# Kernel tuning notes

Measured on AMD Instinct MI355X. Metric: run time of the kernel, lower is better.

The kernel has to match this reference:

```python
import jax, jax.numpy as jnp
import numpy as np

N_NODES = 50000
N_EDGES = 800000
NFEAT, NHID, NCLASS = 512, 128, 40


def setup_inputs() -> dict:
    key = jax.random.key(0)
    ks = jax.random.split(key, 8)
    stdv1 = 1.0 / np.sqrt(NHID)
    stdv2 = 1.0 / np.sqrt(NCLASS)
    x = jax.random.normal(ks[0], (N_NODES, NFEAT), dtype=jnp.float32)
    W1 = jax.random.uniform(ks[1], (NFEAT, NHID), jnp.float32, -stdv1, stdv1)
    b1 = jax.random.uniform(ks[2], (NHID,), jnp.float32, -stdv1, stdv1)
    W2 = jax.random.uniform(ks[3], (NHID, NCLASS), jnp.float32, -stdv2, stdv2)
    b2 = jax.random.uniform(ks[4], (NCLASS,), jnp.float32, -stdv2, stdv2)
    edge_src = jax.random.randint(ks[5], (N_EDGES,), 0, N_NODES, dtype=jnp.int32)
    edge_dst = jax.random.randint(ks[6], (N_EDGES,), 0, N_NODES, dtype=jnp.int32)
    # normalized adjacency weights (positive, ~1/deg scale)
    edge_w = jax.random.uniform(ks[7], (N_EDGES,), jnp.float32, 0.0, 2.0 / 16.0)
    return {"x": x, "W1": W1, "b1": b1, "W2": W2, "b2": b2,
            "edge_src": edge_src, "edge_dst": edge_dst, "edge_w": edge_w}


def _spmm(edge_src, edge_dst, edge_w, support, n_nodes):
    # out[i] = sum_{e: dst(e)=i} w_e * support[src(e)]  == spmm(adj, support)
    msgs = edge_w[:, None] * support[edge_src]          # [E, F]
    return jax.ops.segment_sum(msgs, edge_dst, num_segments=n_nodes)


def reference(x, W1, b1, W2, b2, edge_src, edge_dst, edge_w):
    # layer 1: dense transform then sparse aggregation, bias, relu
    support = x @ W1                                     # [N, nhid]
    h = _spmm(edge_src, edge_dst, edge_w, support, x.shape[0]) + b1
    h = jax.nn.relu(h)
    # dropout is identity in eval mode
    # layer 2
    support2 = h @ W2                                    # [N, nclass]
    out = _spmm(edge_src, edge_dst, edge_w, support2, x.shape[0]) + b2
    return out
```

## Files before the change

kernel.cpp:

```cpp
#include <hip/hip_runtime.h>
#include <hip/hip_bf16.h>


#define NFEAT 512
#define NHID  128
#define NCLS  40
#define BSH   8
#define SLOTSH 6
#define BSLOT 6144
#define ACHUNK 2048

typedef __attribute__((ext_vector_type(8))) short bf16x8;
typedef __attribute__((ext_vector_type(4))) short bf16x4;
typedef __attribute__((ext_vector_type(4))) float f32x4;
typedef __fp16 cvt16x2 __attribute__((ext_vector_type(2)));
typedef _Float16 h16x2 __attribute__((ext_vector_type(2)));

__device__ inline short f2bf(float f) {
  __hip_bfloat16 b = __float2bfloat16(f);
  return *reinterpret_cast<short*>(&b);
}

__device__ inline bf16x8 cvt8(float4 a, float4 b) {
  bf16x8 r;
  r[0] = f2bf(a.x); r[1] = f2bf(a.y); r[2] = f2bf(a.z); r[3] = f2bf(a.w);
  r[4] = f2bf(b.x); r[5] = f2bf(b.y); r[6] = f2bf(b.z); r[7] = f2bf(b.w);
  return r;
}

__device__ inline unsigned pk2u(cvt16x2 v) { union { cvt16x2 h; unsigned u; } x; x.h = v; return x.u; }
__device__ inline cvt16x2 u2h(unsigned u)  { union { cvt16x2 h; unsigned u; } x; x.u = u; return x.h; }
__device__ inline h16x2   u2a(unsigned u)  { union { h16x2 h; unsigned u; } x; x.u = u; return x.h; }

__global__ __launch_bounds__(256) void zero_kernel(int4* __restrict__ p, int n4) {
  int i = blockIdx.x * 256 + threadIdx.x;
  if (i < n4) p[i] = make_int4(0, 0, 0, 0);
}

__global__ __launch_bounds__(256) void bucketize(
    const int* __restrict__ esrc, const int* __restrict__ edst,
    const float* __restrict__ ew, int* __restrict__ bcur,
    int* __restrict__ deg,
    int* __restrict__ bsrc, float* __restrict__ bw, int* __restrict__ bdst,
    int E, int nb) {
  __shared__ int lh[256], lo[256], gbase[256];
  __shared__ int s_src[ACHUNK];
  __shared__ float s_w[ACHUNK];
  __shared__ int s_dst[ACHUNK];
  const int tid = threadIdx.x;
  const int base = blockIdx.x * ACHUNK;
  const int cnt = min(ACHUNK, E - base);

  for (int t = tid; t < nb; t += 256) lh[t] = 0;
  __syncthreads();

  int my_s[8], my_d[8], my_t[8];
  float my_w[8];
#pragma unroll
  for (int i = 0; i < 8; ++i) {
    int idx = base + i * 256 + tid;
    if (idx < E) {
      my_s[i] = esrc[idx];
      my_d[i] = edst[idx];
      my_w[i] = ew[idx];
      my_t[i] = atomicAdd(&lh[my_d[i] >> BSH], 1);
      atomicAdd(&deg[my_d[i]], 1);
    }
  }
  __syncthreads();
  if (tid == 0) {
    int run = 0;
    for (int b = 0; b < nb; ++b) { lo[b] = run; run += lh[b]; }
  }
  __syncthreads();
  if (tid < nb && lh[tid] > 0)
    gbase[tid] = tid * BSLOT + atomicAdd(&bcur[tid], lh[tid]);
  __syncthreads();
#pragma unroll
  for (int i = 0; i < 8; ++i) {
    int idx = base + i * 256 + tid;
    if (idx < E) {
      int p = lo[my_d[i] >> BSH] + my_t[i];
      s_src[p] = my_s[i];
      s_w[p] = my_w[i];
      s_dst[p] = my_d[i];
    }
  }
  __syncthreads();
  for (int j = tid; j < cnt; j += 256) {
    int d = s_dst[j];
    int b = d >> BSH;
    int g = gbase[b] + (j - lo[b]);
    bsrc[g] = s_src[j];
    bw[g] = s_w[j];
    bdst[g] = d;
  }
}

__global__ __launch_bounds__(256) void bucket_scatter(
    const int* __restrict__ bcur, const int* __restrict__ bsrc,
    const float* __restrict__ bw, const int* __restrict__ bdst,
    int2* __restrict__ cwsrc, int n) {
  __shared__ int cur[1 << BSH];
  const int tid = threadIdx.x;
  const int d0 = blockIdx.x << BSH;
  for (int t = tid; t < (1 << BSH); t += 256) cur[t] = (d0 + t) << SLOTSH;
  __syncthreads();
  const int bstart = blockIdx.x * BSLOT;
  const int bend = bstart + bcur[blockIdx.x];
  for (int j = bstart + tid; j < bend; j += 256) {
    int d = bdst[j];
    int slot = atomicAdd(&cur[d - d0], 1);
    float w = bw[j];
    cwsrc[slot] = make_int2(bsrc[j], (int)pk2u(__builtin_amdgcn_cvt_pkrtz(w, w)));
  }
}

__global__ __launch_bounds__(256) void w1t_kernel(
    const float* __restrict__ W1, __hip_bfloat16* __restrict__ W1t) {
  __shared__ float t[64][129];
  const int tid = threadIdx.x;
  const int k0 = blockIdx.x * 64;
#pragma unroll
  for (int i = 0; i < 8; ++i) {
    int f = i * 256 + tid;
    int r = f >> 5, c = (f & 31) << 2;
    float4 v = *(const float4*)&W1[(size_t)(k0 + r) * NHID + c];
    t[r][c] = v.x; t[r][c + 1] = v.y; t[r][c + 2] = v.z; t[r][c + 3] = v.w;
  }
  __syncthreads();
#pragma unroll
  for (int i = 0; i < 32; ++i) {
    int o = i * 256 + tid;
    int k = o & 63, n = o >> 6;
    W1t[(size_t)n * NFEAT + k0 + k] = __float2bfloat16(t[k][n]);
  }
}

__global__ __launch_bounds__(256, 3) void gemm1_mfma(
    const float* __restrict__ x, const __hip_bfloat16* __restrict__ W1t,
    _Float16* __restrict__ support, int nrows) {
  __shared__ __align__(16) char sA[2][64 * 64 * 2];
  __shared__ __align__(16) char sB[2][128 * 64 * 2];
  const int tid = threadIdx.x;
  const int lane = tid & 63;
  const int wid = tid >> 6;
  const int wm = wid >> 1, wn = wid & 1;
  const int row0 = blockIdx.x * 64;
  const int l15 = lane & 15, l4 = lane >> 4;

  const int s_ar = tid >> 2;
  const int s_ac = (tid & 3) * 16;
  const int s_br = tid >> 1;
  const int s_bc = (tid & 1) * 32;
  const bool a_ok = (row0 + s_ar) < nrows;
  const float* aptr = &x[(size_t)(row0 + s_ar) * NFEAT + s_ac];
  const uint4* bptr = (const uint4*)&W1t[(size_t)s_br * NFEAT + s_bc];

  f32x4 acc[2][4];
#pragma unroll
  for (int m = 0; m < 2; ++m)
#pragma unroll
    for (int n = 0; n < 4; ++n) acc[m][n] = (f32x4){0.f, 0.f, 0.f, 0.f};

  float4 ra0[4], ra1[4];
  uint4 rb0[4], rb1[4];

  auto LOADAB = [&](int kt, int sel) {
    if (sel == 0) {
      if (a_ok) {
        const float4* p = (const float4*)(aptr + (size_t)kt * 64);
#pragma unroll
        for (int i = 0; i < 4; ++i) ra0[i] = p[i];
      } else {
        float4 z = make_float4(0.f, 0.f, 0.f, 0.f);
#pragma unroll
        for (int i = 0; i < 4; ++i) ra0[i] = z;
      }
      const uint4* q = bptr + (size_t)kt * 8;
#pragma unroll
      for (int i = 0; i < 4; ++i) rb0[i] = q[i];
    } else {
      if (a_ok) {
        const float4* p = (const float4*)(aptr + (size_t)kt * 64);
#pragma unroll
        for (int i = 0; i < 4; ++i) ra1[i] = p[i];
      } else {
        float4 z = make_float4(0.f, 0.f, 0.f, 0.f);
#pragma unroll
        for (int i = 0; i < 4; ++i) ra1[i] = z;
      }
      const uint4* q = bptr + (size_t)kt * 8;
#pragma unroll
      for (int i = 0; i < 4; ++i) rb1[i] = q[i];
    }
  };
  auto WRITE = [&](int buf, int sel) {
    bf16x8 c0, c1;
    if (sel == 0) { c0 = cvt8(ra0[0], ra0[1]); c1 = cvt8(ra0[2], ra0[3]); }
    else          { c0 = cvt8(ra1[0], ra1[1]); c1 = cvt8(ra1[2], ra1[3]); }
    int swa = (s_ar & 7) << 4;
    *(bf16x8*)(sA[buf] + ((s_ar * 128 + s_ac * 2) ^ swa)) = c0;
    *(bf16x8*)(sA[buf] + ((s_ar * 128 + s_ac * 2 + 16) ^ swa)) = c1;
    int swb = (s_br & 7) << 4;
#pragma unroll
    for (int i = 0; i < 4; ++i) {
      uint4 v = (sel == 0) ? rb0[i] : rb1[i];
      *(uint4*)(sB[buf] + ((s_br * 128 + s_bc * 2 + i * 16) ^ swb)) = v;
    }
  };
  auto COMP = [&](int buf) {
#pragma unroll
    for (int kk = 0; kk < 64; kk += 32) {
      bf16x8 a[2], b[4];
      int cb = (kk + l4 * 8) * 2;
#pragma unroll
      for (int m = 0; m < 2; ++m) {
        int r = wm * 32 + m * 16 + l15;
        a[m] = *(const bf16x8*)(sA[buf] + ((r * 128 + cb) ^ ((r & 7) << 4)));
      }
#pragma unroll
      for (int n = 0; n < 4; ++n) {
        int r = wn * 64 + n * 16 + l15;
        b[n] = *(const bf16x8*)(sB[buf] + ((r * 128 + cb) ^ ((r & 7) << 4)));
      }
#pragma unroll
      for (int m = 0; m < 2; ++m)
#pragma unroll
        for (int n = 0; n < 4; ++n)
          acc[m][n] = __builtin_amdgcn_mfma_f32_16x16x32_bf16(a[m], b[n], acc[m][n], 0, 0, 0);
    }
  };
  auto BAR = [&]() {
    asm volatile("s_waitcnt lgkmcnt(0)" ::: "memory");
    __builtin_amdgcn_sched_barrier(0);
    __builtin_amdgcn_s_barrier();
    __builtin_amdgcn_sched_barrier(0);
  };

  LOADAB(0, 0);
  LOADAB(1, 1);
  WRITE(0, 0);
  LOADAB(2, 0);
  BAR();

#pragma unroll
  for (int t = 0; t < 8; ++t) {
    if (t < 7) {
      if ((t + 1) & 1) {
        WRITE(1, 1);
        if (t + 3 < 8) LOADAB(t + 3, 1);
      } else {
        WRITE(0, 0);
        if (t + 3 < 8) LOADAB(t + 3, 0);
      }
    }
    COMP(t & 1);
    if (t < 7) BAR();
  }

#pragma unroll
  for (int m = 0; m < 2; ++m) {
#pragma unroll
    for (int r = 0; r < 4; ++r) {
      int grow = row0 + wm * 32 + m * 16 + l4 * 4 + r;
      if (grow < nrows) {
#pragma unroll
        for (int n = 0; n < 4; ++n) {
          int col = wn * 64 + n * 16 + l15;
          support[(size_t)grow * NHID + col] = (_Float16)acc[m][n][r];
        }
      }
    }
  }
}

__global__ __launch_bounds__(256) void spmm1_fused(
    const int* __restrict__ deg, const int2* __restrict__ cwsrc,
    const _Float16* __restrict__ support, const float* __restrict__ b1,
    const float* __restrict__ W2, _Float16* __restrict__ s2, int n) {
  __shared__ unsigned swt2[64 * 40];
  __shared__ unsigned shh2[4][64];
  const int tid = threadIdx.x;
  for (int i = tid; i < 64 * 40; i += 256) {
    int k2 = i / 40, c = i - k2 * 40;
    swt2[i] = pk2u(__builtin_amdgcn_cvt_pkrtz(W2[(2 * k2) * NCLS + c],
                                              W2[(2 * k2 + 1) * NCLS + c]));
  }
  __syncthreads();

  const int w = tid >> 6;
  const int f2 = tid & 63;
  const int node = blockIdx.x * 4 + w;
  if (node >= n) return;
  const int dg = deg[node];
  int2 eself = (f2 < dg) ? cwsrc[(node << SLOTSH) + f2] : make_int2(0, 0);
  h16x2 accA = (h16x2){(_Float16)0, (_Float16)0};
  h16x2 accB = (h16x2){(_Float16)0, (_Float16)0};
  const unsigned* sp = (const unsigned*)support;
  int j = 0;
  for (; j + 7 < dg; j += 8) {
#pragma unroll
    for (int q = 0; q < 8; ++q) {
      int s = __builtin_amdgcn_readlane(eself.x, j + q);
      unsigned w2u = (unsigned)__builtin_amdgcn_readlane(eself.y, j + q);
      const unsigned* rowp = sp + ((size_t)(unsigned)s << 6);
      unsigned u = rowp[f2];
      if (q & 1) accB += u2a(u) * u2a(w2u);
      else       accA += u2a(u) * u2a(w2u);
    }
  }
  for (; j < dg; ++j) {
    int s = __builtin_amdgcn_readlane(eself.x, j);
    unsigned w2u = (unsigned)__builtin_amdgcn_readlane(eself.y, j);
    const unsigned* rowp = sp + ((size_t)(unsigned)s << 6);
    unsigned u = rowp[f2];
    if (j & 1) accB += u2a(u) * u2a(w2u);
    else       accA += u2a(u) * u2a(w2u);
  }
  h16x2 acc2 = accA + accB;
  float a0 = fmaxf((float)acc2[0] + b1[f2 * 2], 0.f);
  float a1 = fmaxf((float)acc2[1] + b1[f2 * 2 + 1], 0.f);
  shh2[w][f2] = pk2u(__builtin_amdgcn_cvt_pkrtz(a0, a1));
  if (f2 < NCLS) {
    float acc = 0.f;
#pragma unroll 8
    for (int k2 = 0; k2 < 64; ++k2)
      acc = __builtin_amdgcn_fdot2(u2h(shh2[w][k2]), u2h(swt2[k2 * 40 + f2]), acc, false);
    s2[(size_t)node * NCLS + f2] = (_Float16)acc;
  }
}

__global__ __launch_bounds__(256) void spmm2_gather(
    const int* __restrict__ deg, const int2* __restrict__ cwsrc,
    const _Float16* __restrict__ s2,
    const float* __restrict__ b2, float* __restrict__ out, int n) {
  const int w = threadIdx.x >> 6;
  const int f2 = threadIdx.x & 63;
  const int node = blockIdx.x * 4 + w;
  if (node >= n) return;
  const int dg = deg[node];
  int2 eself = (f2 < dg) ? cwsrc[(node << SLOTSH) + f2] : make_int2(0, 0);
  const unsigned f2c = (f2 < 20) ? (unsigned)f2 : 0u;
  h16x2 accA = (h16x2){(_Float16)0, (_Float16)0};
  h16x2 accB = (h16x2){(_Float16)0, (_Float16)0};
  const unsigned* sp = (const unsigned*)s2;
  int j = 0;
  for (; j + 7 < dg; j += 8) {
#pragma unroll
    for (int q = 0; q < 8; ++q) {
      int s = __builtin_amdgcn_readlane(eself.x, j + q);
      unsigned w2u = (unsigned)__builtin_amdgcn_readlane(eself.y, j + q);
      unsigned u = sp[(size_t)(unsigned)s * 20u + f2c];
      if (q & 1) accB += u2a(u) * u2a(w2u);
      else       accA += u2a(u) * u2a(w2u);
    }
  }
  for (; j < dg; ++j) {
    int s = __builtin_amdgcn_readlane(eself.x, j);
    unsigned w2u = (unsigned)__builtin_amdgcn_readlane(eself.y, j);
    unsigned u = sp[(size_t)(unsigned)s * 20u + f2c];
    if (j & 1) accB += u2a(u) * u2a(w2u);
    else       accA += u2a(u) * u2a(w2u);
  }
  if (f2 < 20) {
    h16x2 acc2 = accA + accB;
    float2 o;
    o.x = (float)acc2[0] + b2[f2 * 2];
    o.y = (float)acc2[1] + b2[f2 * 2 + 1];
    *(float2*)&out[(size_t)node * NCLS + f2 * 2] = o;
  }
}

extern "C" void kernel_launch(void* const* d_in, const int* in_sizes, int n_in,
                              void* d_out, int out_size, void* d_ws, size_t ws_size,
                              hipStream_t stream) {
  const float* x   = (const float*)d_in[0];
  const float* W1  = (const float*)d_in[1];
  const float* b1  = (const float*)d_in[2];
  const float* W2  = (const float*)d_in[3];
  const float* b2  = (const float*)d_in[4];
  const int* esrc  = (const int*)d_in[5];
  const int* edst  = (const int*)d_in[6];
  const float* ew  = (const float*)d_in[7];
  float* out = (float*)d_out;

  const int N = in_sizes[0] / NFEAT;
  const int E = in_sizes[5];
  const int NB = (N + (1 << BSH) - 1) >> BSH;

  char* ws = (char*)d_ws;
  size_t off = 0;
  auto alloc = [&](size_t bytes) {
    void* p = ws + off;
    off += (bytes + 255) & ~(size_t)255;
    return p;
  };
  int2*  cwsrc = (int2*)alloc((size_t)N * (1 << SLOTSH) * 8);
  int*   degb  = (int*)alloc((size_t)((N + NB + 3) & ~3) * 4);
  int*   deg   = degb;
  int*   bcur  = degb + N;
  int*   bsrc  = (int*)alloc((size_t)NB * BSLOT * 4);
  float* bw    = (float*)alloc((size_t)NB * BSLOT * 4);
  int*   bdst  = (int*)alloc((size_t)NB * BSLOT * 4);
  __hip_bfloat16* W1t = (__hip_bfloat16*)alloc((size_t)NHID * NFEAT * 2);
  _Float16* support   = (_Float16*)alloc((size_t)N * NHID * 2);
  _Float16* s2        = (_Float16*)alloc((size_t)N * NCLS * 2);

  const int nz4 = (N + NB + 3) / 4;
  zero_kernel<<<(nz4 + 255) / 256, 256, 0, stream>>>((int4*)degb, nz4);
  bucketize<<<(E + ACHUNK - 1) / ACHUNK, 256, 0, stream>>>(
      esrc, edst, ew, bcur, deg, bsrc, bw, bdst, E, NB);
  bucket_scatter<<<NB, 256, 0, stream>>>(bcur, bsrc, bw, bdst, cwsrc, N);

  w1t_kernel<<<NFEAT / 64, 256, 0, stream>>>(W1, W1t);
  gemm1_mfma<<<(N + 63) / 64, 256, 0, stream>>>(x, W1t, support, N);
  spmm1_fused<<<(N + 3) / 4, 256, 0, stream>>>(deg, cwsrc, support, b1, W2, s2, N);

  spmm2_gather<<<(N + 3) / 4, 256, 0, stream>>>(deg, cwsrc, s2, b2, out, N);
}
```

Baseline: 174.7 us.

## Merge GEMM1 with bucketize, fuse W1 transpose with zeroing, MFMA for layer-2 transform

Folds the W1 transpose and workspace zeroing into one launch. Runs the dense x@W1 GEMM and edge bucketization as disjoint block ranges of a single kernel so the bandwidth-bound GEMM and the atomic-heavy bucketing can overlap. spmm1 now handles 16 nodes per block and does the h@W2 product with bf16 MFMA instead of per-lane fdot2 loops, which also amortizes the W2 load into shared memory. The risks are larger shared-memory use in the fused kernel, which may lower occupancy, and bf16 instead of fp16 precision for the hidden activations.

```diff
diff --git a/kernel.cpp b/kernel.cpp
--- a/kernel.cpp
+++ b/kernel.cpp
@@ -11,7 +11,6 @@
 #define ACHUNK 2048
 
 typedef __attribute__((ext_vector_type(8))) short bf16x8;
-typedef __attribute__((ext_vector_type(4))) short bf16x4;
 typedef __attribute__((ext_vector_type(4))) float f32x4;
 typedef __fp16 cvt16x2 __attribute__((ext_vector_type(2)));
 typedef _Float16 h16x2 __attribute__((ext_vector_type(2)));
@@ -29,26 +28,190 @@
 }
 
 __device__ inline unsigned pk2u(cvt16x2 v) { union { cvt16x2 h; unsigned u; } x; x.h = v; return x.u; }
-__device__ inline cvt16x2 u2h(unsigned u)  { union { cvt16x2 h; unsigned u; } x; x.u = u; return x.h; }
 __device__ inline h16x2   u2a(unsigned u)  { union { h16x2 h; unsigned u; } x; x.u = u; return x.h; }
 
-__global__ __launch_bounds__(256) void zero_kernel(int4* __restrict__ p, int n4) {
-  int i = blockIdx.x * 256 + threadIdx.x;
-  if (i < n4) p[i] = make_int4(0, 0, 0, 0);
-}
-
-__global__ __launch_bounds__(256) void bucketize(
-    const int* __restrict__ esrc, const int* __restrict__ edst,
-    const float* __restrict__ ew, int* __restrict__ bcur,
-    int* __restrict__ deg,
+__global__ __launch_bounds__(256) void w1t_zero(
+    const float* __restrict__ W1, __hip_bfloat16* __restrict__ W1t,
+    int4* __restrict__ zp, int n4) {
+  __shared__ float t[64][129];
+  const int tid = threadIdx.x;
+  if (blockIdx.x < 8) {
+    const int k0 = blockIdx.x * 64;
+#pragma unroll
+    for (int i = 0; i < 8; ++i) {
+      int f = i * 256 + tid;
+      int r = f >> 5, c = (f & 31) << 2;
+      float4 v = *(const float4*)&W1[(size_t)(k0 + r) * NHID + c];
+      t[r][c] = v.x; t[r][c + 1] = v.y; t[r][c + 2] = v.z; t[r][c + 3] = v.w;
+    }
+    __syncthreads();
+#pragma unroll
+    for (int i = 0; i < 32; ++i) {
+      int o = i * 256 + tid;
+      int k = o & 63, n = o >> 6;
+      W1t[(size_t)n * NFEAT + k0 + k] = __float2bfloat16(t[k][n]);
+    }
+  } else {
+    int i = (blockIdx.x - 8) * 256 + tid;
+    if (i < n4) zp[i] = make_int4(0, 0, 0, 0);
+  }
+}
+
+__device__ __forceinline__ void gemm1_body(
+    char* smem, const float* __restrict__ x, const __hip_bfloat16* __restrict__ W1t,
+    _Float16* __restrict__ support, int nrows, int bid) {
+  char* sA0 = smem;
+  char* sB0 = smem + 16384;
+  const int tid = threadIdx.x;
+  const int lane = tid & 63;
+  const int wid = tid >> 6;
+  const int wm = wid >> 1, wn = wid & 1;
+  const int row0 = bid * 64;
+  const int l15 = lane & 15, l4 = lane >> 4;
+
+  const int s_ar = tid >> 2;
+  const int s_ac = (tid & 3) * 16;
+  const int s_br = tid >> 1;
+  const int s_bc = (tid & 1) * 32;
+  const bool a_ok = (row0 + s_ar) < nrows;
+  const float* aptr = &x[(size_t)(row0 + s_ar) * NFEAT + s_ac];
+  const uint4* bptr = (const uint4*)&W1t[(size_t)s_br * NFEAT + s_bc];
+
+  f32x4 acc[2][4];
+#pragma unroll
+  for (int m = 0; m < 2; ++m)
+#pragma unroll
+    for (int n = 0; n < 4; ++n) acc[m][n] = (f32x4){0.f, 0.f, 0.f, 0.f};
+
+  float4 ra0[4], ra1[4];
+  uint4 rb0[4], rb1[4];
+
+  auto LOADAB = [&](int kt, int sel) {
+    if (sel == 0) {
+      if (a_ok) {
+        const float4* p = (const float4*)(aptr + (size_t)kt * 64);
+#pragma unroll
+        for (int i = 0; i < 4; ++i) ra0[i] = p[i];
+      } else {
+        float4 z = make_float4(0.f, 0.f, 0.f, 0.f);
+#pragma unroll
+        for (int i = 0; i < 4; ++i) ra0[i] = z;
+      }
+      const uint4* q = bptr + (size_t)kt * 8;
+#pragma unroll
+      for (int i = 0; i < 4; ++i) rb0[i] = q[i];
+    } else {
+      if (a_ok) {
+        const float4* p = (const float4*)(aptr + (size_t)kt * 64);
+#pragma unroll
+        for (int i = 0; i < 4; ++i) ra1[i] = p[i];
+      } else {
+        float4 z = make_float4(0.f, 0.f, 0.f, 0.f);
+#pragma unroll
+        for (int i = 0; i < 4; ++i) ra1[i] = z;
+      }
+      const uint4* q = bptr + (size_t)kt * 8;
+#pragma unroll
+      for (int i = 0; i < 4; ++i) rb1[i] = q[i];
+    }
+  };
+  auto WRITE = [&](int buf, int sel) {
+    bf16x8 c0, c1;
+    if (sel == 0) { c0 = cvt8(ra0[0], ra0[1]); c1 = cvt8(ra0[2], ra0[3]); }
+    else          { c0 = cvt8(ra1[0], ra1[1]); c1 = cvt8(ra1[2], ra1[3]); }
+    int swa = (s_ar & 7) << 4;
+    char* sA = sA0 + buf * 8192;
+    *(bf16x8*)(sA + ((s_ar * 128 + s_ac * 2) ^ swa)) = c0;
+    *(bf16x8*)(sA + ((s_ar * 128 + s_ac * 2 + 16) ^ swa)) = c1;
+    int swb = (s_br & 7) << 4;
+    char* sB = sB0 + buf * 16384;
+#pragma unroll
+    for (int i = 0; i < 4; ++i) {
+      uint4 v = (sel == 0) ? rb0[i] : rb1[i];
+      *(uint4*)(sB + ((s_br * 128 + s_bc * 2 + i * 16) ^ swb)) = v;
+    }
+  };
+  auto COMP = [&](int buf) {
+    char* sA = sA0 + buf * 8192;
+    char* sB = sB0 + buf * 16384;
+#pragma unroll
+    for (int kk = 0; kk < 64; kk += 32) {
+      bf16x8 a[2], b[4];
+      int cb = (kk + l4 * 8) * 2;
+#pragma unroll
+      for (int m = 0; m < 2; ++m) {
+        int r = wm * 32 + m * 16 + l15;
+        a[m] = *(const bf16x8*)(sA + ((r * 128 + cb) ^ ((r & 7) << 4)));
+      }
+#pragma unroll
+      for (int n = 0; n < 4; ++n) {
+        int r = wn * 64 + n * 16 + l15;
+        b[n] = *(const bf16x8*)(sB + ((r * 128 + cb) ^ ((r & 7) << 4)));
+      }
+#pragma unroll
+      for (int m = 0; m < 2; ++m)
+#pragma unroll
+        for (int n = 0; n < 4; ++n)
+          acc[m][n] = __builtin_amdgcn_mfma_f32_16x16x32_bf16(a[m], b[n], acc[m][n], 0, 0, 0);
+    }
+  };
+  auto BAR = [&]() {
+    asm volatile("s_waitcnt lgkmcnt(0)" ::: "memory");
+    __builtin_amdgcn_sched_barrier(0);
+    __builtin_amdgcn_s_barrier();
+    __builtin_amdgcn_sched_barrier(0);
+  };
+
+  LOADAB(0, 0);
+  LOADAB(1, 1);
+  WRITE(0, 0);
+  LOADAB(2, 0);
+  BAR();
+
+#pragma unroll
+  for (int t = 0; t < 8; ++t) {
+    if (t < 7) {
+      if ((t + 1) & 1) {
+        WRITE(1, 1);
+        if (t + 3 < 8) LOADAB(t + 3, 1);
+      } else {
+        WRITE(0, 0);
+        if (t + 3 < 8) LOADAB(t + 3, 0);
+      }
+    }
+    COMP(t & 1);
+    if (t < 7) BAR();
+  }
+
+#pragma unroll
+  for (int m = 0; m < 2; ++m) {
+#pragma unroll
+    for (int r = 0; r < 4; ++r) {
+      int grow = row0 + wm * 32 + m * 16 + l4 * 4 + r;
+      if (grow < nrows) {
+#pragma unroll
+        for (int n = 0; n < 4; ++n) {
+          int col = wn * 64 + n * 16 + l15;
+          support[(size_t)grow * NHID + col] = (_Float16)acc[m][n][r];
+        }
+      }
+    }
+  }
+}
+
+__device__ __forceinline__ void bucketize_body(
+    char* smem, const int* __restrict__ esrc, const int* __restrict__ edst,
+    const float* __restrict__ ew, int* __restrict__ bcur, int* __restrict__ deg,
     int* __restrict__ bsrc, float* __restrict__ bw, int* __restrict__ bdst,
-    int E, int nb) {
-  __shared__ int lh[256], lo[256], gbase[256];
-  __shared__ int s_src[ACHUNK];
-  __shared__ float s_w[ACHUNK];
-  __shared__ int s_dst[ACHUNK];
+    int E, int nb, int bid) {
+  int* lh = (int*)smem;
+  int* lo = lh + 256;
+  int* gbase = lo + 256;
+  int* s_src = gbase + 256;
+  float* s_w = (float*)(s_src + ACHUNK);
+  int* s_dst = (int*)(s_w + ACHUNK);
   const int tid = threadIdx.x;
-  const int base = blockIdx.x * ACHUNK;
+  const int base = bid * ACHUNK;
   const int cnt = min(ACHUNK, E - base);
 
   for (int t = tid; t < nb; t += 256) lh[t] = 0;
@@ -97,6 +260,21 @@
   }
 }
 
+__global__ __launch_bounds__(256, 3) void fat_kernel(
+    const float* __restrict__ x, const __hip_bfloat16* __restrict__ W1t,
+    _Float16* __restrict__ support, int nrows, int gemmBlocks,
+    const int* __restrict__ esrc, const int* __restrict__ edst,
+    const float* __restrict__ ew, int* __restrict__ bcur, int* __restrict__ deg,
+    int* __restrict__ bsrc, float* __restrict__ bw, int* __restrict__ bdst,
+    int E, int nb) {
+  __shared__ __align__(16) char smem[49152];
+  if ((int)blockIdx.x < gemmBlocks)
+    gemm1_body(smem, x, W1t, support, nrows, blockIdx.x);
+  else
+    bucketize_body(smem, esrc, edst, ew, bcur, deg, bsrc, bw, bdst, E, nb,
+                   blockIdx.x - gemmBlocks);
+}
+
 __global__ __launch_bounds__(256) void bucket_scatter(
     const int* __restrict__ bcur, const int* __restrict__ bsrc,
     const float* __restrict__ bw, const int* __restrict__ bdst,
@@ -116,218 +294,78 @@
   }
 }
 
-__global__ __launch_bounds__(256) void w1t_kernel(
-    const float* __restrict__ W1, __hip_bfloat16* __restrict__ W1t) {
-  __shared__ float t[64][129];
-  const int tid = threadIdx.x;
-  const int k0 = blockIdx.x * 64;
-#pragma unroll
-  for (int i = 0; i < 8; ++i) {
-    int f = i * 256 + tid;
-    int r = f >> 5, c = (f & 31) << 2;
-    float4 v = *(const float4*)&W1[(size_t)(k0 + r) * NHID + c];
-    t[r][c] = v.x; t[r][c + 1] = v.y; t[r][c + 2] = v.z; t[r][c + 3] = v.w;
-  }
-  __syncthreads();
-#pragma unroll
-  for (int i = 0; i < 32; ++i) {
-    int o = i * 256 + tid;
-    int k = o & 63, n = o >> 6;
-    W1t[(size_t)n * NFEAT + k0 + k] = __float2bfloat16(t[k][n]);
-  }
-}
-
-__global__ __launch_bounds__(256, 3) void gemm1_mfma(
-    const float* __restrict__ x, const __hip_bfloat16* __restrict__ W1t,
-    _Float16* __restrict__ support, int nrows) {
-  __shared__ __align__(16) char sA[2][64 * 64 * 2];
-  __shared__ __align__(16) char sB[2][128 * 64 * 2];
-  const int tid = threadIdx.x;
-  const int lane = tid & 63;
-  const int wid = tid >> 6;
-  const int wm = wid >> 1, wn = wid & 1;
-  const int row0 = blockIdx.x * 64;
-  const int l15 = lane & 15, l4 = lane >> 4;
-
-  const int s_ar = tid >> 2;
-  const int s_ac = (tid & 3) * 16;
-  const int s_br = tid >> 1;
-  const int s_bc = (tid & 1) * 32;
-  const bool a_ok = (row0 + s_ar) < nrows;
-  const float* aptr = &x[(size_t)(row0 + s_ar) * NFEAT + s_ac];
-  const uint4* bptr = (const uint4*)&W1t[(size_t)s_br * NFEAT + s_bc];
-
-  f32x4 acc[2][4];
-#pragma unroll
-  for (int m = 0; m < 2; ++m)
-#pragma unroll
-    for (int n = 0; n < 4; ++n) acc[m][n] = (f32x4){0.f, 0.f, 0.f, 0.f};
-
-  float4 ra0[4], ra1[4];
-  uint4 rb0[4], rb1[4];
-
-  auto LOADAB = [&](int kt, int sel) {
-    if (sel == 0) {
-      if (a_ok) {
-        const float4* p = (const float4*)(aptr + (size_t)kt * 64);
-#pragma unroll
-        for (int i = 0; i < 4; ++i) ra0[i] = p[i];
-      } else {
-        float4 z = make_float4(0.f, 0.f, 0.f, 0.f);
-#pragma unroll
-        for (int i = 0; i < 4; ++i) ra0[i] = z;
-      }
-      const uint4* q = bptr + (size_t)kt * 8;
-#pragma unroll
-      for (int i = 0; i < 4; ++i) rb0[i] = q[i];
-    } else {
-      if (a_ok) {
-        const float4* p = (const float4*)(aptr + (size_t)kt * 64);
-#pragma unroll
-        for (int i = 0; i < 4; ++i) ra1[i] = p[i];
-      } else {
-        float4 z = make_float4(0.f, 0.f, 0.f, 0.f);
-#pragma unroll
-        for (int i = 0; i < 4; ++i) ra1[i] = z;
-      }
-      const uint4* q = bptr + (size_t)kt * 8;
-#pragma unroll
-      for (int i = 0; i < 4; ++i) rb1[i] = q[i];
-    }
-  };
-  auto WRITE = [&](int buf, int sel) {
-    bf16x8 c0, c1;
-    if (sel == 0) { c0 = cvt8(ra0[0], ra0[1]); c1 = cvt8(ra0[2], ra0[3]); }
-    else          { c0 = cvt8(ra1[0], ra1[1]); c1 = cvt8(ra1[2], ra1[3]); }
-    int swa = (s_ar & 7) << 4;
-    *(bf16x8*)(sA[buf] + ((s_ar * 128 + s_ac * 2) ^ swa)) = c0;
-    *(bf16x8*)(sA[buf] + ((s_ar * 128 + s_ac * 2 + 16) ^ swa)) = c1;
-    int swb = (s_br & 7) << 4;
-#pragma unroll
-    for (int i = 0; i < 4; ++i) {
-      uint4 v = (sel == 0) ? rb0[i] : rb1[i];
-      *(uint4*)(sB[buf] + ((s_br * 128 + s_bc * 2 + i * 16) ^ swb)) = v;
-    }
-  };
-  auto COMP = [&](int buf) {
-#pragma unroll
-    for (int kk = 0; kk < 64; kk += 32) {
-      bf16x8 a[2], b[4];
-      int cb = (kk + l4 * 8) * 2;
-#pragma unroll
-      for (int m = 0; m < 2; ++m) {
-        int r = wm * 32 + m * 16 + l15;
-        a[m] = *(const bf16x8*)(sA[buf] + ((r * 128 + cb) ^ ((r & 7) << 4)));
-      }
-#pragma unroll
-      for (int n = 0; n < 4; ++n) {
-        int r = wn * 64 + n * 16 + l15;
-        b[n] = *(const bf16x8*)(sB[buf] + ((r * 128 + cb) ^ ((r & 7) << 4)));
-      }
-#pragma unroll
-      for (int m = 0; m < 2; ++m)
-#pragma unroll
-        for (int n = 0; n < 4; ++n)
-          acc[m][n] = __builtin_amdgcn_mfma_f32_16x16x32_bf16(a[m], b[n], acc[m][n], 0, 0, 0);
-    }
-  };
-  auto BAR = [&]() {
-    asm volatile("s_waitcnt lgkmcnt(0)" ::: "memory");
-    __builtin_amdgcn_sched_barrier(0);
-    __builtin_amdgcn_s_barrier();
-    __builtin_amdgcn_sched_barrier(0);
-  };
-
-  LOADAB(0, 0);
-  LOADAB(1, 1);
-  WRITE(0, 0);
-  LOADAB(2, 0);
-  BAR();
-
-#pragma unroll
-  for (int t = 0; t < 8; ++t) {
-    if (t < 7) {
-      if ((t + 1) & 1) {
-        WRITE(1, 1);
-        if (t + 3 < 8) LOADAB(t + 3, 1);
-      } else {
-        WRITE(0, 0);
-        if (t + 3 < 8) LOADAB(t + 3, 0);
-      }
-    }
-    COMP(t & 1);
-    if (t < 7) BAR();
-  }
-
-#pragma unroll
-  for (int m = 0; m < 2; ++m) {
-#pragma unroll
-    for (int r = 0; r < 4; ++r) {
-      int grow = row0 + wm * 32 + m * 16 + l4 * 4 + r;
-      if (grow < nrows) {
-#pragma unroll
-        for (int n = 0; n < 4; ++n) {
-          int col = wn * 64 + n * 16 + l15;
-          support[(size_t)grow * NHID + col] = (_Float16)acc[m][n][r];
-        }
-      }
-    }
-  }
-}
-
 __global__ __launch_bounds__(256) void spmm1_fused(
     const int* __restrict__ deg, const int2* __restrict__ cwsrc,
     const _Float16* __restrict__ support, const float* __restrict__ b1,
     const float* __restrict__ W2, _Float16* __restrict__ s2, int n) {
-  __shared__ unsigned swt2[64 * 40];
-  __shared__ unsigned shh2[4][64];
+  __shared__ __align__(16) char sW[48 * 128 * 2];
+  __shared__ __align__(16) char sH[16 * 128 * 2];
   const int tid = threadIdx.x;
-  for (int i = tid; i < 64 * 40; i += 256) {
-    int k2 = i / 40, c = i - k2 * 40;
-    swt2[i] = pk2u(__builtin_amdgcn_cvt_pkrtz(W2[(2 * k2) * NCLS + c],
-                                              W2[(2 * k2 + 1) * NCLS + c]));
-  }
-  __syncthreads();
-
-  const int w = tid >> 6;
-  const int f2 = tid & 63;
-  const int node = blockIdx.x * 4 + w;
-  if (node >= n) return;
-  const int dg = deg[node];
-  int2 eself = (f2 < dg) ? cwsrc[(node << SLOTSH) + f2] : make_int2(0, 0);
-  h16x2 accA = (h16x2){(_Float16)0, (_Float16)0};
-  h16x2 accB = (h16x2){(_Float16)0, (_Float16)0};
+  for (int i = tid; i < 48 * 128; i += 256) {
+    int nn = i >> 7, k = i & 127;
+    float v = (nn < NCLS) ? W2[k * NCLS + nn] : 0.f;
+    int byte = (nn * 256 + k * 2) ^ ((nn & 7) << 4);
+    *(short*)(sW + byte) = f2bf(v);
+  }
+
+  const int wv = tid >> 6, f2 = tid & 63;
+  const int node0 = blockIdx.x * 16;
+  const float2 bb = *(const float2*)&b1[f2 * 2];
   const unsigned* sp = (const unsigned*)support;
-  int j = 0;
-  for (; j + 7 < dg; j += 8) {
-#pragma unroll
-    for (int q = 0; q < 8; ++q) {
-      int s = __builtin_amdgcn_readlane(eself.x, j + q);
-      unsigned w2u = (unsigned)__builtin_amdgcn_readlane(eself.y, j + q);
-      const unsigned* rowp = sp + ((size_t)(unsigned)s << 6);
-      unsigned u = rowp[f2];
-      if (q & 1) accB += u2a(u) * u2a(w2u);
+#pragma unroll
+  for (int nn = 0; nn < 4; ++nn) {
+    const int node = node0 + wv * 4 + nn;
+    const int dg = (node < n) ? deg[node] : 0;
+    int2 eself = (f2 < dg) ? cwsrc[((size_t)node << SLOTSH) + f2] : make_int2(0, 0);
+    h16x2 accA = (h16x2){(_Float16)0, (_Float16)0};
+    h16x2 accB = (h16x2){(_Float16)0, (_Float16)0};
+    int j = 0;
+    for (; j + 7 < dg; j += 8) {
+#pragma unroll
+      for (int q = 0; q < 8; ++q) {
+        int s = __builtin_amdgcn_readlane(eself.x, j + q);
+        unsigned w2u = (unsigned)__builtin_amdgcn_readlane(eself.y, j + q);
+        unsigned u = sp[((size_t)(unsigned)s << 6) | (unsigned)f2];
+        if (q & 1) accB += u2a(u) * u2a(w2u);
+        else       accA += u2a(u) * u2a(w2u);
+      }
+    }
+    for (; j < dg; ++j) {
+      int s = __builtin_amdgcn_readlane(eself.x, j);
+      unsigned w2u = (unsigned)__builtin_amdgcn_readlane(eself.y, j);
+      unsigned u = sp[((size_t)(unsigned)s << 6) | (unsigned)f2];
+      if (j & 1) accB += u2a(u) * u2a(w2u);
       else       accA += u2a(u) * u2a(w2u);
     }
-  }
-  for (; j < dg; ++j) {
-    int s = __builtin_amdgcn_readlane(eself.x, j);
-    unsigned w2u = (unsigned)__builtin_amdgcn_readlane(eself.y, j);
-    const unsigned* rowp = sp + ((size_t)(unsigned)s << 6);
-    unsigned u = rowp[f2];
-    if (j & 1) accB += u2a(u) * u2a(w2u);
-    else       accA += u2a(u) * u2a(w2u);
-  }
-  h16x2 acc2 = accA + accB;
-  float a0 = fmaxf((float)acc2[0] + b1[f2 * 2], 0.f);
-  float a1 = fmaxf((float)acc2[1] + b1[f2 * 2 + 1], 0.f);
-  shh2[w][f2] = pk2u(__builtin_amdgcn_cvt_pkrtz(a0, a1));
-  if (f2 < NCLS) {
-    float acc = 0.f;
-#pragma unroll 8
-    for (int k2 = 0; k2 < 64; ++k2)
-      acc = __builtin_amdgcn_fdot2(u2h(shh2[w][k2]), u2h(swt2[k2 * 40 + f2]), acc, false);
-    s2[(size_t)node * NCLS + f2] = (_Float16)acc;
+    h16x2 acc2 = accA + accB;
+    float a0 = fmaxf((float)acc2[0] + bb.x, 0.f);
+    float a1 = fmaxf((float)acc2[1] + bb.y, 0.f);
+    int row = wv * 4 + nn;
+    int byte = (row * 256 + f2 * 4) ^ ((row & 7) << 4);
+    unsigned pair = (unsigned)(unsigned short)f2bf(a0) |
+                    ((unsigned)(unsigned short)f2bf(a1) << 16);
+    *(unsigned*)(sH + byte) = pair;
+  }
+  __syncthreads();
+  if (wv < 3) {
+    const int l15 = f2 & 15, l4 = f2 >> 4;
+    f32x4 acc = (f32x4){0.f, 0.f, 0.f, 0.f};
+#pragma unroll
+    for (int kk = 0; kk < 4; ++kk) {
+      int ka = (kk * 32 + l4 * 8) * 2;
+      bf16x8 af = *(const bf16x8*)(sH + ((l15 * 256 + ka) ^ ((l15 & 7) << 4)));
+      int nrow = wv * 16 + l15;
+      bf16x8 bf = *(const bf16x8*)(sW + ((nrow * 256 + ka) ^ ((nrow & 7) << 4)));
+      acc = __builtin_amdgcn_mfma_f32_16x16x32_bf16(af, bf, acc, 0, 0, 0);
+    }
+    int col = wv * 16 + l15;
+    if (col < NCLS) {
+#pragma unroll
+      for (int r = 0; r < 4; ++r) {
+        int node = node0 + l4 * 4 + r;
+        if (node < n) s2[(size_t)node * NCLS + col] = (_Float16)acc[r];
+      }
+    }
   }
 }
 
@@ -340,7 +378,7 @@
   const int node = blockIdx.x * 4 + w;
   if (node >= n) return;
   const int dg = deg[node];
-  int2 eself = (f2 < dg) ? cwsrc[(node << SLOTSH) + f2] : make_int2(0, 0);
+  int2 eself = (f2 < dg) ? cwsrc[((size_t)node << SLOTSH) + f2] : make_int2(0, 0);
   const unsigned f2c = (f2 < 20) ? (unsigned)f2 : 0u;
   h16x2 accA = (h16x2){(_Float16)0, (_Float16)0};
   h16x2 accB = (h16x2){(_Float16)0, (_Float16)0};
@@ -408,14 +446,17 @@
   _Float16* s2        = (_Float16*)alloc((size_t)N * NCLS * 2);
 
   const int nz4 = (N + NB + 3) / 4;
-  zero_kernel<<<(nz4 + 255) / 256, 256, 0, stream>>>((int4*)degb, nz4);
-  bucketize<<<(E + ACHUNK - 1) / ACHUNK, 256, 0, stream>>>(
+  w1t_zero<<<8 + (nz4 + 255) / 256, 256, 0, stream>>>(W1, W1t, (int4*)degb, nz4);
+
+  const int GEMMB = (N + 63) / 64;
+  const int BUCKB = (E + ACHUNK - 1) / ACHUNK;
+  fat_kernel<<<GEMMB + BUCKB, 256, 0, stream>>>(
+      x, W1t, support, N, GEMMB,
       esrc, edst, ew, bcur, deg, bsrc, bw, bdst, E, NB);
+
   bucket_scatter<<<NB, 256, 0, stream>>>(bcur, bsrc, bw, bdst, cwsrc, N);
 
-  w1t_kernel<<<NFEAT / 64, 256, 0, stream>>>(W1, W1t);
-  gemm1_mfma<<<(N + 63) / 64, 256, 0, stream>>>(x, W1t, support, N);
-  spmm1_fused<<<(N + 3) / 4, 256, 0, stream>>>(deg, cwsrc, support, b1, W2, s2, N);
+  spmm1_fused<<<(N + 15) / 16, 256, 0, stream>>>(deg, cwsrc, support, b1, W2, s2, N);
 
   spmm2_gather<<<(N + 3) / 4, 256, 0, stream>>>(deg, cwsrc, s2, b2, out, N);
 }
```

Result: faster. 169.7 us (-2.9%).
